# Performance work log

Measured on AMD Instinct MI355X. Metric: run time of the kernel, lower is better.

The kernel has to match this reference:

```python
import jax, jax.numpy as jnp
import numpy as np

EPS = 1e-8
TOP_K = 2


def _l2norm(v, axis=-1):
    # F.normalize: v / max(||v||_2, eps)
    n = jnp.sqrt(jnp.sum(v * v, axis=axis, keepdims=True))
    return v / jnp.maximum(n, EPS)


def setup_inputs() -> dict:
    key = jax.random.key(0)
    ks = jax.random.split(key, 5)
    B, S, D, F, E = 2, 2048, 512, 2048, 8
    x = jax.random.normal(ks[0], (B, S, D), dtype=jnp.float32)
    anchors = jax.random.normal(ks[1], (E, D), dtype=jnp.float32)
    W1 = jax.random.normal(ks[2], (E, D, F), dtype=jnp.float32) * (1.0 / np.sqrt(D))
    b1 = jnp.zeros((E, F), dtype=jnp.float32)
    W2 = jax.random.normal(ks[3], (E, F, D), dtype=jnp.float32) * (1.0 / np.sqrt(F))
    b2 = jnp.zeros((E, D), dtype=jnp.float32)
    return {"x": x, "anchors": anchors, "W1": W1, "b1": b1, "W2": W2, "b2": b2}


def reference(x, anchors, W1, b1, W2, b2):
    B, S, D = x.shape
    E = anchors.shape[0]
    x_flat = x.reshape(B * S, D)  # (T, D)

    # Semantic resonance routing: cosine similarity with anchors
    x_n = _l2norm(x_flat)
    a_n = _l2norm(anchors)
    scores = jnp.einsum('td,ed->te', x_n, a_n)  # (T, E)

    # Noisy top-k (eval mode: no noise) + softmax gates over top-k scores
    topk_scores, topk_idx = jax.lax.top_k(scores, TOP_K)  # (T, K)
    gates = jax.nn.softmax(topk_scores, axis=-1)  # (T, K)

    # Combine weights per (token, expert); top-k indices are distinct per token
    T = B * S
    combine = jnp.zeros((T, E), dtype=x.dtype)
    combine = combine.at[jnp.arange(T)[:, None], topk_idx].add(gates)

    # Per-expert MLP (Linear -> exact GELU -> Linear), combined by gates.
    # Dense-over-experts form is mathematically identical to the sorted
    # grouped dispatch + index_add in the original module.
    h = jnp.einsum('td,edf->tef', x_flat, W1) + b1[None]  # (T, E, F)
    h = jax.nn.gelu(h, approximate=False)
    y = jnp.einsum('tef,efd->ted', h, W2) + b2[None]  # (T, E, D)
    out_flat = jnp.einsum('te,ted->td', combine, y)  # (T, D)

    out = out_flat.reshape(B, S, D)
    # aux_data equivalents: anchors_norm, resonance_scores, topk_indices
    return out, a_n, scores, topk_idx
```

## Files before the change

kernel.cpp:

```cpp
#include <hip/hip_runtime.h>
#include <cstdint>


#define T_TOK 4096
#define D_DIM 512
#define F_DIM 2048
#define E_EXP 8
#define NROWS 9216
#define MAXTILES 72

typedef __bf16 bf16x8 __attribute__((ext_vector_type(8)));
typedef float  f32x4  __attribute__((ext_vector_type(4)));
typedef unsigned short u16;

__device__ __forceinline__ u16 f2b(float f) {
    return __builtin_bit_cast(unsigned short, (__bf16)f);
}
__device__ __forceinline__ void gload16(void* lds, const void* g) {
    __builtin_amdgcn_global_load_lds(
        (const __attribute__((address_space(1))) void*)g,
        (__attribute__((address_space(3))) void*)lds, 16, 0, 0);
}

__global__ void init_k(int* __restrict__ cnt, int* __restrict__ rowmap,
                       float* __restrict__ rowgate, float* __restrict__ outacc) {
    int tid = blockIdx.x * 256 + threadIdx.x;
    int nth = gridDim.x * 256;
    if (tid < E_EXP) cnt[tid] = 0;
    for (int i = tid; i < NROWS; i += nth) { rowmap[i] = -1; rowgate[i] = 0.f; }
    float4* o4 = (float4*)outacc;
    for (int i = tid; i < (T_TOK * D_DIM) / 4; i += nth)
        o4[i] = float4{0.f, 0.f, 0.f, 0.f};
}

__global__ void anchors_k(const float* __restrict__ anchors,
                          float* __restrict__ an, float* __restrict__ dout_an) {
    int tid = threadIdx.x;
    int lane = tid & 63, e = tid >> 6;
    const float4* ar = (const float4*)(anchors + e * D_DIM + lane * 8);
    float4 v0 = ar[0], v1 = ar[1];
    float ss = v0.x*v0.x + v0.y*v0.y + v0.z*v0.z + v0.w*v0.w
             + v1.x*v1.x + v1.y*v1.y + v1.z*v1.z + v1.w*v1.w;
#pragma unroll
    for (int off = 32; off >= 1; off >>= 1) ss += __shfl_xor(ss, off, 64);
    float inv = 1.0f / fmaxf(sqrtf(ss), 1e-8f);
    float o[8] = {v0.x*inv, v0.y*inv, v0.z*inv, v0.w*inv,
                  v1.x*inv, v1.y*inv, v1.z*inv, v1.w*inv};
#pragma unroll
    for (int i = 0; i < 8; ++i) {
        an[e * D_DIM + lane * 8 + i] = o[i];
        dout_an[e * D_DIM + lane * 8 + i] = o[i];
    }
}

__global__ void routing_k(const float* __restrict__ x, const float* __restrict__ an,
                          float* __restrict__ dout_scores, float* __restrict__ dout_idx,
                          int* __restrict__ idxs, float* __restrict__ gates,
                          int* __restrict__ cnt) {
    __shared__ float anl[E_EXP * 544];
    __shared__ int hist[E_EXP];
    int tid = threadIdx.x;
    if (tid < E_EXP) hist[tid] = 0;
    for (int i = tid; i < E_EXP * D_DIM; i += 256) {
        int e = i >> 9, d = i & 511;
        anl[e * 544 + (d >> 7) * 136 + (d & 127)] = an[i];
    }
    __syncthreads();

    int p = tid & 3;
    int tok = blockIdx.x * 64 + (tid >> 2);
    const float4* xr = (const float4*)(x + (size_t)tok * D_DIM + p * 128);
    const float* ab = &anl[p * 136];
    float dot[E_EXP] = {};
    float ss = 0.f;
    for (int c = 0; c < 32; ++c) {
        float4 xv = xr[c];
        ss += xv.x*xv.x + xv.y*xv.y + xv.z*xv.z + xv.w*xv.w;
#pragma unroll
        for (int e = 0; e < E_EXP; ++e) {
            float4 av = *(const float4*)&ab[e * 544 + c * 4];
            dot[e] += xv.x*av.x + xv.y*av.y + xv.z*av.z + xv.w*av.w;
        }
    }
#pragma unroll
    for (int off = 1; off <= 2; off <<= 1) {
        ss += __shfl_xor(ss, off, 64);
#pragma unroll
        for (int e = 0; e < E_EXP; ++e) dot[e] += __shfl_xor(dot[e], off, 64);
    }

    if (p == 0) {
        float inv = 1.0f / fmaxf(sqrtf(ss), 1e-8f);
        float s[E_EXP];
#pragma unroll
        for (int e = 0; e < E_EXP; ++e) s[e] = dot[e] * inv;
        int i0 = 0; float b0 = s[0];
#pragma unroll
        for (int e = 1; e < E_EXP; ++e) if (s[e] > b0) { b0 = s[e]; i0 = e; }
        int i1 = -1; float b1v = -1e30f;
#pragma unroll
        for (int e = 0; e < E_EXP; ++e)
            if (e != i0 && s[e] > b1v) { b1v = s[e]; i1 = e; }
        if (i1 < 0) { i1 = (i0 + 1) & 7; b1v = s[i1]; }
        float g0 = 1.0f / (1.0f + expf(b1v - b0));
        float g1 = 1.0f - g0;
#pragma unroll
        for (int e = 0; e < E_EXP; ++e) dout_scores[tok * E_EXP + e] = s[e];
        dout_idx[tok * 2 + 0] = (float)i0;
        dout_idx[tok * 2 + 1] = (float)i1;
        idxs[tok * 2 + 0] = i0; idxs[tok * 2 + 1] = i1;
        gates[tok * 2 + 0] = g0; gates[tok * 2 + 1] = g1;
        atomicAdd(&hist[i0], 1);
        atomicAdd(&hist[i1], 1);
    }
    __syncthreads();
    if (tid < E_EXP) atomicAdd(&cnt[tid], hist[tid]);
}

__global__ void offs_k(const int* __restrict__ cnt, int* __restrict__ offs,
                       int* __restrict__ cur) {
    if (threadIdx.x == 0 && blockIdx.x == 0) {
        int acc = 0;
        for (int e = 0; e < E_EXP; ++e) {
            offs[e] = acc; cur[e] = acc;
            acc += (cnt[e] + 127) & ~127;
        }
        offs[E_EXP] = acc;
    }
}

__global__ void assign_k(const int* __restrict__ idxs, const float* __restrict__ gates,
                         int* __restrict__ cur, int* __restrict__ rowmap,
                         float* __restrict__ rowgate) {
    int t = blockIdx.x * 256 + threadIdx.x;
    if (t >= T_TOK) return;
#pragma unroll
    for (int k = 0; k < 2; ++k) {
        int e = idxs[t * 2 + k];
        e = min(max(e, 0), E_EXP - 1);
        int r = atomicAdd(&cur[e], 1);
        if (r >= 0 && r < NROWS) {
            rowmap[r] = t;
            rowgate[r] = gates[t * 2 + k];
        }
    }
}

__global__ void gather_k(const float* __restrict__ x, const int* __restrict__ rowmap,
                         u16* __restrict__ Xg) {
    int r = blockIdx.x;
    int t = rowmap[r];
    int c = threadIdx.x * 2;
    ushort2 o;
    if (t < 0 || t >= T_TOK) { o.x = 0; o.y = 0; }
    else {
        float2 v = *(const float2*)(x + (size_t)t * D_DIM + c);
        o.x = f2b(v.x); o.y = f2b(v.y);
    }
    *(ushort2*)(Xg + (size_t)r * D_DIM + c) = o;
}

__global__ void transpose_cast_k(const float* __restrict__ in, u16* __restrict__ out,
                                 int R, int C) {
    size_t zoff = (size_t)blockIdx.z * R * C;
    in += zoff; out += zoff;
    __shared__ float t[64][65];
    int c0 = blockIdx.x * 64, r0 = blockIdx.y * 64;
    int tid = threadIdx.x;
    int cq = tid & 15, rb = tid >> 4;
#pragma unroll
    for (int pass = 0; pass < 4; ++pass) {
        int rr = rb + pass * 16;
        float4 v = *(const float4*)(in + (size_t)(r0 + rr) * C + c0 + cq * 4);
        t[rr][cq * 4 + 0] = v.x; t[rr][cq * 4 + 1] = v.y;
        t[rr][cq * 4 + 2] = v.z; t[rr][cq * 4 + 3] = v.w;
    }
    __syncthreads();
    int rg = tid & 15, cb = tid >> 4;
#pragma unroll
    for (int pass = 0; pass < 4; ++pass) {
        int c = cb + pass * 16;
        ushort4 o;
        o.x = f2b(t[rg * 4 + 0][c]); o.y = f2b(t[rg * 4 + 1][c]);
        o.z = f2b(t[rg * 4 + 2][c]); o.w = f2b(t[rg * 4 + 3][c]);
        *(ushort4*)(out + (size_t)(c0 + c) * R + r0 + rg * 4) = o;
    }
}

template <int MODE>
__launch_bounds__(256, 2)
__global__ void gemm_k(const u16* __restrict__ A, int lda,
                       const u16* __restrict__ BtBase, int ldb,
                       u16* __restrict__ Hout, const float* __restrict__ b1,
                       float* __restrict__ outacc,
                       const int* __restrict__ rowmap, const float* __restrict__ rowgate,
                       const int* __restrict__ offs, int kPer) {
    int row0 = blockIdx.y * 128;
    if (row0 >= offs[E_EXP]) return;
    int e = 0;
#pragma unroll
    for (int i = 1; i < E_EXP; ++i) if (row0 >= offs[i]) e = i;
    const u16* Bt = BtBase + (size_t)e * D_DIM * F_DIM;
    int n0 = blockIdx.x * 128;
    int k_begin = (MODE == 1) ? (int)blockIdx.z * kPer : 0;
    int k_end = k_begin + kPer;

    alignas(16) __shared__ u16 As[128 * 64];
    alignas(16) __shared__ u16 Bs[128 * 64];

    int tid = threadIdx.x;
    int lane = tid & 63;
    int wv = tid >> 6;
    int wm = wv & 1, wn = wv >> 1;
    int kq = lane >> 4;
    int l15 = lane & 15;

    const u16* aSrc[4]; const u16* bSrc[4];
    u16* aDst[4]; u16* bDst[4];
#pragma unroll
    for (int i = 0; i < 4; ++i) {
        int slot = i * 256 + tid;
        int m = slot >> 3;
        int kc = (slot & 7) ^ (m & 7);
        aSrc[i] = A + (size_t)(row0 + m) * lda + kc * 8;
        bSrc[i] = Bt + (size_t)(n0 + m) * ldb + kc * 8;
        aDst[i] = As + slot * 8;
        bDst[i] = Bs + slot * 8;
    }

    f32x4 acc[4][4];
#pragma unroll
    for (int i = 0; i < 4; ++i)
#pragma unroll
        for (int j = 0; j < 4; ++j) acc[i][j] = f32x4{0.f, 0.f, 0.f, 0.f};

    for (int k0 = k_begin; k0 < k_end; k0 += 64) {
#pragma unroll
        for (int i = 0; i < 4; ++i) gload16(aDst[i], aSrc[i] + k0);
#pragma unroll
        for (int i = 0; i < 4; ++i) gload16(bDst[i], bSrc[i] + k0);
        asm volatile("s_waitcnt vmcnt(0)" ::: "memory");
        __syncthreads();
#pragma unroll
        for (int kk = 0; kk < 2; ++kk) {
            int kc = kk * 4 + kq;
            bf16x8 af[4], bfr[4];
#pragma unroll
            for (int i = 0; i < 4; ++i) {
                int rowA = wm * 64 + i * 16 + l15;
                af[i] = *(const bf16x8*)(As + rowA * 64 + ((kc ^ (rowA & 7)) * 8));
                int rowB = wn * 64 + i * 16 + l15;
                bfr[i] = *(const bf16x8*)(Bs + rowB * 64 + ((kc ^ (rowB & 7)) * 8));
            }
#pragma unroll
            for (int i = 0; i < 4; ++i)
#pragma unroll
                for (int j = 0; j < 4; ++j)
                    acc[i][j] = __builtin_amdgcn_mfma_f32_16x16x32_bf16(
                        af[i], bfr[j], acc[i][j], 0, 0, 0);
        }
        __syncthreads();
    }

    if constexpr (MODE == 0) {
        const float* b1e = b1 + (size_t)e * F_DIM;
#pragma unroll
        for (int i = 0; i < 4; ++i) {
            int gr = row0 + wm * 64 + i * 16 + kq * 4;
#pragma unroll
            for (int j = 0; j < 4; ++j) {
                int gc = n0 + wn * 64 + j * 16 + l15;
                float bb = b1e[gc];
#pragma unroll
                for (int r = 0; r < 4; ++r) {
                    float v = acc[i][j][r] + bb;
                    float h = 0.5f * v * (1.0f + erff(v * 0.70710678118f));
                    Hout[(size_t)(gr + r) * F_DIM + gc] = f2b(h);
                }
            }
        }
    } else {
#pragma unroll
        for (int i = 0; i < 4; ++i) {
            int grb = row0 + wm * 64 + i * 16 + kq * 4;
#pragma unroll
            for (int r = 0; r < 4; ++r) {
                int tok = rowmap[grb + r];
                float g = rowgate[grb + r];
                if (tok >= 0 && tok < T_TOK) {
                    float* orow = outacc + (size_t)tok * D_DIM;
#pragma unroll
                    for (int j = 0; j < 4; ++j) {
                        int gc = n0 + wn * 64 + j * 16 + l15;
                        atomicAdd(orow + gc, g * acc[i][j][r]);
                    }
                }
            }
        }
    }
}

__global__ void final_k(const float* __restrict__ outacc, const int* __restrict__ idxs,
                        const float* __restrict__ gates, const float* __restrict__ b2,
                        float* __restrict__ dout) {
    int t = blockIdx.x;
    int i0 = min(max(idxs[t * 2], 0), E_EXP - 1);
    int i1 = min(max(idxs[t * 2 + 1], 0), E_EXP - 1);
    float g0 = gates[t * 2], g1 = gates[t * 2 + 1];
    int d = threadIdx.x * 2;
    float2 oa = *(const float2*)(outacc + (size_t)t * D_DIM + d);
    const float* p0 = b2 + (size_t)i0 * D_DIM + d;
    const float* p1 = b2 + (size_t)i1 * D_DIM + d;
    float2 o;
    o.x = oa.x + g0 * p0[0] + g1 * p1[0];
    o.y = oa.y + g0 * p0[1] + g1 * p1[1];
    *(float2*)(dout + (size_t)t * D_DIM + d) = o;
}

#define OFF_AN      0u
#define OFF_CNT     0x10000u
#define OFF_OFFS    0x10100u
#define OFF_CUR     0x10200u
#define OFF_IDX     0x20000u
#define OFF_GATE    0x28000u
#define OFF_ROWMAP  0x30000u
#define OFF_ROWGATE 0x40000u
#define OFF_OUTACC  0x50000u
#define OFF_XG      0x900000u
#define OFF_W1T     0x1200000u
#define OFF_W2T     0x2200000u
#define OFF_HG      0x3200000u

extern "C" void kernel_launch(void* const* d_in, const int* in_sizes, int n_in,
                              void* d_out, int out_size, void* d_ws, size_t ws_size,
                              hipStream_t stream) {
    const float* x       = (const float*)d_in[0];
    const float* anchors = (const float*)d_in[1];
    const float* W1      = (const float*)d_in[2];
    const float* b1      = (const float*)d_in[3];
    const float* W2      = (const float*)d_in[4];
    const float* b2      = (const float*)d_in[5];
    float* out = (float*)d_out;

    char* ws = (char*)d_ws;
    float* an      = (float*)(ws + OFF_AN);
    int*   cnt     = (int*)(ws + OFF_CNT);
    int*   offs    = (int*)(ws + OFF_OFFS);
    int*   cur     = (int*)(ws + OFF_CUR);
    int*   idxs    = (int*)(ws + OFF_IDX);
    float* gates   = (float*)(ws + OFF_GATE);
    int*   rowmap  = (int*)(ws + OFF_ROWMAP);
    float* rowgate = (float*)(ws + OFF_ROWGATE);
    float* outacc  = (float*)(ws + OFF_OUTACC);
    u16*   Xg      = (u16*)(ws + OFF_XG);
    u16*   W1T     = (u16*)(ws + OFF_W1T);
    u16*   W2T     = (u16*)(ws + OFF_W2T);
    u16*   Hg      = (u16*)(ws + OFF_HG);

    float* out_main   = out;
    float* out_an     = out + (size_t)T_TOK * D_DIM;
    float* out_scores = out_an + E_EXP * D_DIM;
    float* out_idx    = out_scores + (size_t)T_TOK * E_EXP;

    init_k<<<512, 256, 0, stream>>>(cnt, rowmap, rowgate, outacc);
    anchors_k<<<1, 512, 0, stream>>>(anchors, an, out_an);
    routing_k<<<T_TOK / 64, 256, 0, stream>>>(x, an, out_scores, out_idx,
                                              idxs, gates, cnt);
    offs_k<<<1, 64, 0, stream>>>(cnt, offs, cur);
    assign_k<<<T_TOK / 256, 256, 0, stream>>>(idxs, gates, cur, rowmap, rowgate);
    gather_k<<<NROWS, 256, 0, stream>>>(x, rowmap, Xg);
    transpose_cast_k<<<dim3(F_DIM / 64, D_DIM / 64, E_EXP), 256, 0, stream>>>(
        W1, W1T, D_DIM, F_DIM);
    transpose_cast_k<<<dim3(D_DIM / 64, F_DIM / 64, E_EXP), 256, 0, stream>>>(
        W2, W2T, F_DIM, D_DIM);
    gemm_k<0><<<dim3(F_DIM / 128, MAXTILES, 1), 256, 0, stream>>>(
        Xg, D_DIM, W1T, D_DIM, Hg, b1, nullptr, rowmap, nullptr, offs, D_DIM);
    gemm_k<1><<<dim3(D_DIM / 128, MAXTILES, 2), 256, 0, stream>>>(
        Hg, F_DIM, W2T, F_DIM, nullptr, nullptr, outacc, rowmap, rowgate,
        offs, F_DIM / 2);
    final_k<<<T_TOK, 256, 0, stream>>>(outacc, idxs, gates, b2, out_main);
}
```

Baseline: 277.8 us.

## Fuse bias into second GEMM, use tanh GELU, drop LDS swizzle

Removes the final_k pass by zeroing the output buffer directly and adding the b2 bias, scaled by the gate, inside the second GEMM's atomic epilogue on the first K-split only. Replaces the exact erf GELU with the tanh approximation using __expf, which is cheaper but does not match the reference's exact GELU. Also drops the XOR swizzle on the LDS tile layout, which risks more LDS bank conflicts on the fragment reads.

```diff
diff --git a/kernel.cpp b/kernel.cpp
--- a/kernel.cpp
+++ b/kernel.cpp
@@ -21,14 +21,19 @@
         (const __attribute__((address_space(1))) void*)g,
         (__attribute__((address_space(3))) void*)lds, 16, 0, 0);
 }
+__device__ __forceinline__ float gelu_f(float v) {
+    float z = 0.7978845608f * (v + 0.044715f * v * v * v);
+    float t = 1.0f - 2.0f / (1.0f + __expf(2.0f * z));
+    return 0.5f * v * (1.0f + t);
+}
 
 __global__ void init_k(int* __restrict__ cnt, int* __restrict__ rowmap,
-                       float* __restrict__ rowgate, float* __restrict__ outacc) {
+                       float* __restrict__ rowgate, float* __restrict__ outm) {
     int tid = blockIdx.x * 256 + threadIdx.x;
     int nth = gridDim.x * 256;
     if (tid < E_EXP) cnt[tid] = 0;
     for (int i = tid; i < NROWS; i += nth) { rowmap[i] = -1; rowgate[i] = 0.f; }
-    float4* o4 = (float4*)outacc;
+    float4* o4 = (float4*)outm;
     for (int i = tid; i < (T_TOK * D_DIM) / 4; i += nth)
         o4[i] = float4{0.f, 0.f, 0.f, 0.f};
 }
@@ -192,7 +197,7 @@
 __global__ void gemm_k(const u16* __restrict__ A, int lda,
                        const u16* __restrict__ BtBase, int ldb,
                        u16* __restrict__ Hout, const float* __restrict__ b1,
-                       float* __restrict__ outacc,
+                       float* __restrict__ outm, const float* __restrict__ b2,
                        const int* __restrict__ rowmap, const float* __restrict__ rowgate,
                        const int* __restrict__ offs, int kPer) {
     int row0 = blockIdx.y * 128;
@@ -221,7 +226,7 @@
     for (int i = 0; i < 4; ++i) {
         int slot = i * 256 + tid;
         int m = slot >> 3;
-        int kc = (slot & 7) ^ (m & 7);
+        int kc = slot & 7;
         aSrc[i] = A + (size_t)(row0 + m) * lda + kc * 8;
         bSrc[i] = Bt + (size_t)(n0 + m) * ldb + kc * 8;
         aDst[i] = As + slot * 8;
@@ -248,9 +253,9 @@
 #pragma unroll
             for (int i = 0; i < 4; ++i) {
                 int rowA = wm * 64 + i * 16 + l15;
-                af[i] = *(const bf16x8*)(As + rowA * 64 + ((kc ^ (rowA & 7)) * 8));
+                af[i] = *(const bf16x8*)(As + rowA * 64 + kc * 8);
                 int rowB = wn * 64 + i * 16 + l15;
-                bfr[i] = *(const bf16x8*)(Bs + rowB * 64 + ((kc ^ (rowB & 7)) * 8));
+                bfr[i] = *(const bf16x8*)(Bs + rowB * 64 + kc * 8);
             }
 #pragma unroll
             for (int i = 0; i < 4; ++i)
@@ -274,12 +279,13 @@
 #pragma unroll
                 for (int r = 0; r < 4; ++r) {
                     float v = acc[i][j][r] + bb;
-                    float h = 0.5f * v * (1.0f + erff(v * 0.70710678118f));
-                    Hout[(size_t)(gr + r) * F_DIM + gc] = f2b(h);
+                    Hout[(size_t)(gr + r) * F_DIM + gc] = f2b(gelu_f(v));
                 }
             }
         }
     } else {
+        const float* b2e = b2 + (size_t)e * D_DIM;
+        bool addBias = (k_begin == 0);
 #pragma unroll
         for (int i = 0; i < 4; ++i) {
             int grb = row0 + wm * 64 + i * 16 + kq * 4;
@@ -288,33 +294,17 @@
                 int tok = rowmap[grb + r];
                 float g = rowgate[grb + r];
                 if (tok >= 0 && tok < T_TOK) {
-                    float* orow = outacc + (size_t)tok * D_DIM;
+                    float* orow = outm + (size_t)tok * D_DIM;
 #pragma unroll
                     for (int j = 0; j < 4; ++j) {
                         int gc = n0 + wn * 64 + j * 16 + l15;
-                        atomicAdd(orow + gc, g * acc[i][j][r]);
+                        float bb = addBias ? b2e[gc] : 0.f;
+                        atomicAdd(orow + gc, g * (acc[i][j][r] + bb));
                     }
                 }
             }
         }
     }
-}
-
-__global__ void final_k(const float* __restrict__ outacc, const int* __restrict__ idxs,
-                        const float* __restrict__ gates, const float* __restrict__ b2,
-                        float* __restrict__ dout) {
-    int t = blockIdx.x;
-    int i0 = min(max(idxs[t * 2], 0), E_EXP - 1);
-    int i1 = min(max(idxs[t * 2 + 1], 0), E_EXP - 1);
-    float g0 = gates[t * 2], g1 = gates[t * 2 + 1];
-    int d = threadIdx.x * 2;
-    float2 oa = *(const float2*)(outacc + (size_t)t * D_DIM + d);
-    const float* p0 = b2 + (size_t)i0 * D_DIM + d;
-    const float* p1 = b2 + (size_t)i1 * D_DIM + d;
-    float2 o;
-    o.x = oa.x + g0 * p0[0] + g1 * p1[0];
-    o.y = oa.y + g0 * p0[1] + g1 * p1[1];
-    *(float2*)(dout + (size_t)t * D_DIM + d) = o;
 }
 
 #define OFF_AN      0u
@@ -325,7 +315,6 @@
 #define OFF_GATE    0x28000u
 #define OFF_ROWMAP  0x30000u
 #define OFF_ROWGATE 0x40000u
-#define OFF_OUTACC  0x50000u
 #define OFF_XG      0x900000u
 #define OFF_W1T     0x1200000u
 #define OFF_W2T     0x2200000u
@@ -351,7 +340,6 @@
     float* gates   = (float*)(ws + OFF_GATE);
     int*   rowmap  = (int*)(ws + OFF_ROWMAP);
     float* rowgate = (float*)(ws + OFF_ROWGATE);
-    float* outacc  = (float*)(ws + OFF_OUTACC);
     u16*   Xg      = (u16*)(ws + OFF_XG);
     u16*   W1T     = (u16*)(ws + OFF_W1T);
     u16*   W2T     = (u16*)(ws + OFF_W2T);
@@ -362,7 +350,7 @@
     float* out_scores = out_an + E_EXP * D_DIM;
     float* out_idx    = out_scores + (size_t)T_TOK * E_EXP;
 
-    init_k<<<512, 256, 0, stream>>>(cnt, rowmap, rowgate, outacc);
+    init_k<<<512, 256, 0, stream>>>(cnt, rowmap, rowgate, out_main);
     anchors_k<<<1, 512, 0, stream>>>(anchors, an, out_an);
     routing_k<<<T_TOK / 64, 256, 0, stream>>>(x, an, out_scores, out_idx,
                                               idxs, gates, cnt);
@@ -374,9 +362,9 @@
     transpose_cast_k<<<dim3(D_DIM / 64, F_DIM / 64, E_EXP), 256, 0, stream>>>(
         W2, W2T, F_DIM, D_DIM);
     gemm_k<0><<<dim3(F_DIM / 128, MAXTILES, 1), 256, 0, stream>>>(
-        Xg, D_DIM, W1T, D_DIM, Hg, b1, nullptr, rowmap, nullptr, offs, D_DIM);
+        Xg, D_DIM, W1T, D_DIM, Hg, b1, nullptr, nullptr,
+        rowmap, nullptr, offs, D_DIM);
     gemm_k<1><<<dim3(D_DIM / 128, MAXTILES, 2), 256, 0, stream>>>(
-        Hg, F_DIM, W2T, F_DIM, nullptr, nullptr, outacc, rowmap, rowgate,
-        offs, F_DIM / 2);
-    final_k<<<T_TOK, 256, 0, stream>>>(outacc, idxs, gates, b2, out_main);
-}
+        Hg, F_DIM, W2T, F_DIM, nullptr, nullptr, out_main, b2,
+        rowmap, rowgate, offs, F_DIM / 2);
+}
```

Measured after the change: 277.8 us. About the same (-0.0%).
